# Optimization experiments

Measured on AMD Instinct MI355X. Metric: run time of the kernel, lower is better.

## Reference

```python
import jax, jax.numpy as jnp
import numpy as np

DIM = 240; NH = 6; HD = 20          # dim, num_heads, head_dim = dim // (2*num_heads)
WS = 16; BWS = 8                    # window size, base window size
R = (WS // BWS) ** 2                # spatial_linear in_features (=4)
LW = WS * WS; LB = BWS * BWS

# static relative-position index for a WSxWS window (same construction as torch buffer)
_coords = np.stack(np.meshgrid(np.arange(WS), np.arange(WS), indexing='ij')).reshape(2, -1)
_rel = (_coords[:, :, None] - _coords[:, None, :]).transpose(1, 2, 0).astype(np.int64)
_rel[..., 0] += WS - 1; _rel[..., 1] += WS - 1; _rel[..., 0] *= 2 * WS - 1
RPI = jnp.asarray(_rel.sum(-1))     # [LW, LW]


def conv2d(x, w, b, pad):
    y = jax.lax.conv_general_dilated(x, w, (1, 1), [(pad, pad), (pad, pad)],
                                     dimension_numbers=('NCHW', 'OIHW', 'NCHW'))
    return y + b[None, :, None, None]


def lrelu(x):
    return jnp.where(x >= 0, x, 0.2 * x)  # LeakyReLU(0.2)


def layer_norm(x, g, b, eps=1e-5):
    m = x.mean(-1, keepdims=True)
    v = jnp.mean((x - m) ** 2, axis=-1, keepdims=True)
    return (x - m) * jax.lax.rsqrt(v + eps) * g + b


def setup_inputs() -> dict:
    key = jax.random.key(0)
    ks = iter(jax.random.split(key, 40))
    rn = lambda shape: jax.random.normal(next(ks), shape, jnp.float32) * 0.02
    B, H, W = 2, 256, 256
    pd = (DIM // 4) // 4  # DynamicPosBias pos_dim = 15
    return {
        'x': jax.random.normal(next(ks), (B, H * W, DIM), jnp.float32),
        # DFE (qv projection)
        'c1_w': rn((DIM // 5, DIM, 1, 1)), 'c1_b': jnp.zeros((DIM // 5,), jnp.float32),
        'c2_w': rn((DIM // 5, DIM // 5, 3, 3)), 'c2_b': jnp.zeros((DIM // 5,), jnp.float32),
        'c3_w': rn((DIM, DIM // 5, 1, 1)), 'c3_b': jnp.zeros((DIM,), jnp.float32),
        'lin_w': rn((DIM, DIM, 1, 1)), 'lin_b': jnp.zeros((DIM,), jnp.float32),
        # spatial linear projection Linear(R, 1)
        'sl_w': rn((1, R)), 'sl_b': jnp.zeros((1,), jnp.float32),
        # DynamicPosBias MLP (residual=False)
        'pp_w': rn((pd, 2)), 'pp_b': jnp.zeros((pd,), jnp.float32),
        'ln1_g': jnp.ones((pd,), jnp.float32), 'ln1_b': jnp.zeros((pd,), jnp.float32),
        'p1_w': rn((pd, pd)), 'p1_b': jnp.zeros((pd,), jnp.float32),
        'ln2_g': jnp.ones((pd,), jnp.float32), 'ln2_b': jnp.zeros((pd,), jnp.float32),
        'p2_w': rn((pd, pd)), 'p2_b': jnp.zeros((pd,), jnp.float32),
        'ln3_g': jnp.ones((pd,), jnp.float32), 'ln3_b': jnp.zeros((pd,), jnp.float32),
        'p3_w': rn((NH, pd)), 'p3_b': jnp.zeros((NH,), jnp.float32),
        # output projection
        'proj_w': rn((DIM, DIM)), 'proj_b': jnp.zeros((DIM,), jnp.float32),
        'H': 256, 'W': 256,
    }


def reference(x, c1_w, c1_b, c2_w, c2_b, c3_w, c3_b, lin_w, lin_b, sl_w, sl_b,
              pp_w, pp_b, ln1_g, ln1_b, p1_w, p1_b, ln2_g, ln2_b, p2_w, p2_b,
              ln3_g, ln3_b, p3_w, p3_b, proj_w, proj_b, H, W):
    B, L, C = x.shape
    # ---- DFE feature projection (conv-gated) ----
    xi = jnp.transpose(x, (0, 2, 1)).reshape(B, C, H, W)
    conv = conv2d(lrelu(conv2d(lrelu(conv2d(xi, c1_w, c1_b, 0)), c2_w, c2_b, 1)), c3_w, c3_b, 0)
    qv = conv * conv2d(xi, lin_w, lin_b, 0)                       # [B,C,H,W]
    qv = jnp.transpose(qv, (0, 2, 3, 1))                          # [B,H,W,C]
    # ---- window partition ----
    nh_w, nw_w = H // WS, W // WS
    qv = qv.reshape(B, nh_w, WS, nw_w, WS, C).transpose(0, 1, 3, 2, 4, 5).reshape(-1, LW, C)
    B_ = qv.shape[0]
    qv = qv.reshape(B_, LW, 2, NH, HD).transpose(2, 0, 3, 1, 4)   # [2,B_,NH,LW,HD]
    q, v = qv[0], qv[1]
    # ---- spatial self-correlation ----
    # spatial linear projection of v: [B_,NH,LW,HD] -> [B_,NH,LB,HD]
    vs = v.reshape(B_, NH, BWS, WS // BWS, BWS, WS // BWS, HD)
    vs = vs.transpose(0, 1, 2, 4, 6, 3, 5).reshape(B_, NH, LB, HD, R)
    vs = jnp.einsum('bnkcr,or->bnkc', vs, sl_w) + sl_b            # Linear(R,1), squeezed
    corr = jnp.einsum('bnlc,bnkc->bnlk', q, vs) / HD              # [B_,NH,LW,LB]
    # dynamic relative position bias (MLP over the mother set of relative coords)
    ph = jnp.arange(1 - WS, WS)
    biases = jnp.stack(jnp.meshgrid(ph, ph, indexing='ij')).reshape(2, -1).T.astype(x.dtype)
    pos = biases @ pp_w.T + pp_b
    pos = jax.nn.relu(layer_norm(pos, ln1_g, ln1_b)) @ p1_w.T + p1_b
    pos = jax.nn.relu(layer_norm(pos, ln2_g, ln2_b)) @ p2_w.T + p2_b
    pos = jax.nn.relu(layer_norm(pos, ln3_g, ln3_b)) @ p3_w.T + p3_b  # [(2*WS-1)^2, NH]
    rpb = jnp.take(pos, RPI.reshape(-1), axis=0).reshape(LW, LW, NH).transpose(2, 0, 1)
    # pool key axis to base-window resolution (consistent with spatial_linear_projection grouping)
    rpb = rpb.reshape(NH, LW, BWS, WS // BWS, BWS, WS // BWS).mean((3, 5)).reshape(NH, LW, LB)
    corr = corr + rpb[None]
    x_s = jnp.einsum('bnlk,bnkc->bnlc', corr, vs)
    x_s = x_s.transpose(0, 2, 1, 3).reshape(B_, LW, NH * HD)      # [B_,LW,C/2]
    # ---- channel self-correlation (single-head over merged channels) ----
    qc = q.transpose(0, 2, 1, 3).reshape(B_, LW, NH * HD)
    vc = v.transpose(0, 2, 1, 3).reshape(B_, LW, NH * HD)
    corr_c = jnp.einsum('blc,bld->bcd', qc, vc) / LW              # [B_,C/2,C/2]
    x_c = jnp.einsum('bcd,bld->blc', corr_c, vc)                  # [B_,LW,C/2]
    # ---- window reverse + spatial-channel fusion ----
    def wrev(t):
        return t.reshape(B, nh_w, nw_w, WS, WS, -1).transpose(0, 1, 3, 2, 4, 5).reshape(B, H, W, -1)
    out = jnp.concatenate([wrev(x_s), wrev(x_c)], axis=-1)        # [B,H,W,C]
    out = out @ proj_w.T + proj_b
    return out.reshape(B, L, C)
```

## Files before the change

### kernel.cpp

```cpp
#include <hip/hip_runtime.h>
#include <math.h>

#define NPIX 131072

typedef __attribute__((ext_vector_type(8))) short bfrag;
typedef __attribute__((ext_vector_type(4))) float facc;
typedef __attribute__((ext_vector_type(4))) unsigned short us4;

__device__ __forceinline__ float lrelu_f(float x) { return x >= 0.f ? x : 0.2f * x; }

__device__ __forceinline__ int pix_of(int w, int l) {
    int b = w >> 8, wi = (w >> 4) & 15, wj = w & 15;
    return ((((b << 4) + wi) * 16 + (l >> 4)) << 8) + (wj << 4) + (l & 15);
}

__device__ __forceinline__ unsigned short bf16rn(float f) {
    unsigned u = __builtin_bit_cast(unsigned, f);
    u += 0x7FFFu + ((u >> 16) & 1u);
    return (unsigned short)(u >> 16);
}
__device__ __forceinline__ float bf16tof(unsigned short h) {
    unsigned u = ((unsigned)h) << 16;
    return __builtin_bit_cast(float, u);
}

__global__ __launch_bounds__(256) void split_x_kernel(const float* __restrict__ x,
                                                      unsigned short* __restrict__ xs2)
{
    int idx = blockIdx.x * 256 + threadIdx.x;
    int row = idx >> 5;
    int k = (idx & 31) * 8;
    float v[8];
    if (k < 240) {
        float4 a = *(const float4*)(x + (size_t)row * 240 + k);
        float4 b = *(const float4*)(x + (size_t)row * 240 + k + 4);
        v[0] = a.x; v[1] = a.y; v[2] = a.z; v[3] = a.w;
        v[4] = b.x; v[5] = b.y; v[6] = b.z; v[7] = b.w;
    } else {
#pragma unroll
        for (int e = 0; e < 8; ++e) v[e] = 0.f;
    }
    bfrag hi, lo;
#pragma unroll
    for (int e = 0; e < 8; ++e) {
        unsigned short h = bf16rn(v[e]);
        hi[e] = (short)h;
        lo[e] = (short)bf16rn(v[e] - bf16tof(h));
    }
    unsigned short* dst = xs2 + (size_t)row * 512 + k;
    *(bfrag*)(dst) = hi;
    *(bfrag*)(dst + 256) = lo;
}

__global__ __launch_bounds__(256) void pack_w_kernel(const float* __restrict__ src,
                                                     int rows, int K,
                                                     unsigned short* __restrict__ dst,
                                                     int total8, int KPAD)
{
    int idx = blockIdx.x * 256 + threadIdx.x;
    if (idx >= total8) return;
    int kper = KPAD >> 3;
    int row = idx / kper;
    int k = (idx - row * kper) * 8;
    float v[8];
#pragma unroll
    for (int e = 0; e < 8; ++e) {
        int kk = k + e;
        v[e] = (row < rows && kk < K) ? src[(size_t)row * K + kk] : 0.f;
    }
    bfrag hi, lo;
#pragma unroll
    for (int e = 0; e < 8; ++e) {
        unsigned short h = bf16rn(v[e]);
        hi[e] = (short)h;
        lo[e] = (short)bf16rn(v[e] - bf16tof(h));
    }
    unsigned short* d = dst + (size_t)row * 2 * KPAD + k;
    *(bfrag*)(d) = hi;
    *(bfrag*)(d + KPAD) = lo;
}

__global__ __launch_bounds__(256) void pack_c2w_kernel(const float* __restrict__ c2_w,
                                                       unsigned short* __restrict__ c2w2)
{
    int idx = blockIdx.x * 256 + threadIdx.x;
    if (idx >= 6912) return;
    int rowid = idx >> 4;
    int c = idx & 15;
    int tap = rowid / 48, n = rowid - tap * 48;
    int ty = tap / 3, tx = tap - ty * 3;
    int lohalf = c >> 3;
    int cbase = (c & 7) * 8;
    bfrag outv;
#pragma unroll
    for (int e = 0; e < 8; ++e) {
        int ci = cbase + e;
        float v = (ci < 48) ? c2_w[(((size_t)n * 48 + ci) * 3 + ty) * 3 + tx] : 0.f;
        unsigned short h = bf16rn(v);
        outv[e] = (short)(lohalf ? bf16rn(v - bf16tof(h)) : h);
    }
    *(bfrag*)(c2w2 + (size_t)rowid * 128 + c * 8) = outv;
}

__device__ __forceinline__ void ln_relu15(const float* h, float* r,
                                          const float* __restrict__ g,
                                          const float* __restrict__ b) {
    float m = 0.f;
#pragma unroll
    for (int f = 0; f < 15; ++f) m += h[f];
    m *= (1.f / 15.f);
    float v = 0.f;
#pragma unroll
    for (int f = 0; f < 15; ++f) { float d = h[f] - m; v += d * d; }
    float rs = rsqrtf(v * (1.f / 15.f) + 1e-5f);
#pragma unroll
    for (int f = 0; f < 15; ++f) {
        float xx = (h[f] - m) * rs * g[f] + b[f];
        r[f] = xx > 0.f ? xx : 0.f;
    }
}

__device__ __forceinline__ void lin15(const float* r, float* h,
                                      const float* __restrict__ w,
                                      const float* __restrict__ b) {
#pragma unroll
    for (int o = 0; o < 15; ++o) {
        float s = b[o];
#pragma unroll
        for (int g = 0; g < 15; ++g) s += r[g] * w[o * 15 + g];
        h[o] = s;
    }
}

__global__ __launch_bounds__(256) void prep_pos_kernel(
    const float* __restrict__ pp_w, const float* __restrict__ pp_b,
    const float* __restrict__ ln1_g, const float* __restrict__ ln1_b,
    const float* __restrict__ p1_w, const float* __restrict__ p1_b,
    const float* __restrict__ ln2_g, const float* __restrict__ ln2_b,
    const float* __restrict__ p2_w, const float* __restrict__ p2_b,
    const float* __restrict__ ln3_g, const float* __restrict__ ln3_b,
    const float* __restrict__ p3_w, const float* __restrict__ p3_b,
    float* __restrict__ pos3)
{
    int tid = threadIdx.x;
    for (int idx = tid; idx < 961; idx += 256) {
        float h[15], r[15];
        float in0 = (float)(idx / 31) - 15.f;
        float in1 = (float)(idx % 31) - 15.f;
#pragma unroll
        for (int f = 0; f < 15; ++f) h[f] = in0 * pp_w[2 * f] + in1 * pp_w[2 * f + 1] + pp_b[f];
        ln_relu15(h, r, ln1_g, ln1_b);
        lin15(r, h, p1_w, p1_b);
        ln_relu15(h, r, ln2_g, ln2_b);
        lin15(r, h, p2_w, p2_b);
        ln_relu15(h, r, ln3_g, ln3_b);
#pragma unroll
        for (int o = 0; o < 6; ++o) {
            float s = p3_b[o];
#pragma unroll
            for (int g = 0; g < 15; ++g) s += r[g] * p3_w[o * 15 + g];
            pos3[idx * 6 + o] = s;
        }
    }
}

__global__ __launch_bounds__(256) void rpb_kernel(const float* __restrict__ pos3,
                                                  float* __restrict__ rpb_t)
{
    int out = blockIdx.x * 256 + threadIdx.x;
    int n = out >> 14;
    int k = (out >> 8) & 63;
    int l = out & 255;
    int a = k >> 3, c = k & 7;
    int i1 = l >> 4, j1 = l & 15;
    float s = 0.f;
#pragma unroll
    for (int bb = 0; bb < 2; ++bb)
#pragma unroll
        for (int d = 0; d < 2; ++d) {
            int i2 = a * 2 + bb, j2 = c * 2 + d;
            int rpi = (i1 - i2 + 15) * 31 + (j1 - j2 + 15);
            s += pos3[rpi * 6 + n];
        }
    rpb_t[out] = s * 0.25f;
}

__device__ __forceinline__ void mfma_kpass3(const unsigned short* __restrict__ A2, int lda2,
                                            const unsigned short* __restrict__ W2, int ldw2,
                                            int ksteps, int mbase, int nbase,
                                            short* lds_a, short* lds_w,
                                            int tid, int wm, int wn,
                                            facc acc[4][4])
{
    int lane = tid & 63;
    int i = lane & 15, g = lane >> 4;
    int kpa = lda2 >> 1, kpw = ldw2 >> 1;
    for (int s = 0; s < ksteps; ++s) {
        int k0 = s * 32;
        {
            int r = tid >> 1, h16 = (tid & 1) * 16;
            const unsigned short* src = A2 + (size_t)(mbase + r) * lda2 + k0 + h16;
            bfrag h0 = *(const bfrag*)(src);
            bfrag h1 = *(const bfrag*)(src + 8);
            bfrag l0 = *(const bfrag*)(src + kpa);
            bfrag l1 = *(const bfrag*)(src + kpa + 8);
            short* dst = lds_a + r * 72 + h16;
            *(bfrag*)(dst)      = h0;  *(bfrag*)(dst + 8)  = h1;
            *(bfrag*)(dst + 32) = l0;  *(bfrag*)(dst + 40) = l1;
        }
        {
            int r = tid >> 1, half = tid & 1;
            const unsigned short* src = W2 + (size_t)(nbase + r) * ldw2 + half * kpw + k0;
            bfrag v0 = *(const bfrag*)(src);
            bfrag v1 = *(const bfrag*)(src + 8);
            bfrag v2 = *(const bfrag*)(src + 16);
            bfrag v3 = *(const bfrag*)(src + 24);
            short* dst = lds_w + r * 72 + half * 32;
            *(bfrag*)(dst)      = v0;  *(bfrag*)(dst + 8)  = v1;
            *(bfrag*)(dst + 16) = v2;  *(bfrag*)(dst + 24) = v3;
        }
        __syncthreads();
        bfrag ah[4], al[4], bh[4], bl[4];
#pragma unroll
        for (int mu = 0; mu < 4; ++mu) {
            const short* p = lds_a + (wm * 64 + mu * 16 + i) * 72 + g * 8;
            ah[mu] = *(const bfrag*)(p);
            al[mu] = *(const bfrag*)(p + 32);
        }
#pragma unroll
        for (int nu = 0; nu < 4; ++nu) {
            const short* p = lds_w + (wn * 64 + nu * 16 + i) * 72 + g * 8;
            bh[nu] = *(const bfrag*)(p);
            bl[nu] = *(const bfrag*)(p + 32);
        }
#pragma unroll
        for (int mu = 0; mu < 4; ++mu)
#pragma unroll
            for (int nu = 0; nu < 4; ++nu) {
                acc[mu][nu] = __builtin_amdgcn_mfma_f32_16x16x32_bf16(ah[mu], bh[nu], acc[mu][nu], 0, 0, 0);
                acc[mu][nu] = __builtin_amdgcn_mfma_f32_16x16x32_bf16(ah[mu], bl[nu], acc[mu][nu], 0, 0, 0);
                acc[mu][nu] = __builtin_amdgcn_mfma_f32_16x16x32_bf16(al[mu], bh[nu], acc[mu][nu], 0, 0, 0);
            }
        __syncthreads();
    }
}

__global__ __launch_bounds__(256) void conv1_mfma_kernel(const unsigned short* __restrict__ xs2,
    const unsigned short* __restrict__ c1_w2, const float* __restrict__ bias,
    unsigned short* __restrict__ t1s)
{
    __shared__ __align__(16) short lds_a[128 * 72];
    __shared__ __align__(16) short lds_w[128 * 72];
    int tid = threadIdx.x;
    int lane = tid & 63, wid = tid >> 6;
    int wm = wid >> 1, wn = wid & 1;
    int mbase = blockIdx.x * 128;
    facc zero = {0.f, 0.f, 0.f, 0.f};
    facc acc[4][4];
#pragma unroll
    for (int mu = 0; mu < 4; ++mu)
#pragma unroll
        for (int nu = 0; nu < 4; ++nu) acc[mu][nu] = zero;

    mfma_kpass3(xs2, 512, c1_w2, 512, 8, mbase, 0, lds_a, lds_w, tid, wm, wn, acc);

    int i = lane & 15, g = lane >> 4;
#pragma unroll
    for (int nu = 0; nu < 4; ++nu) {
        int n = wn * 64 + nu * 16 + i;
        if (n < 48) {
            float bv = bias[n];
#pragma unroll
            for (int mu = 0; mu < 4; ++mu)
#pragma unroll
                for (int rr = 0; rr < 4; ++rr) {
                    size_t m = (size_t)mbase + wm * 64 + mu * 16 + g * 4 + rr;
                    float v = lrelu_f(acc[mu][nu][rr] + bv);
                    unsigned short h = bf16rn(v);
                    t1s[m * 128 + n] = h;
                    t1s[m * 128 + 64 + n] = bf16rn(v - bf16tof(h));
                }
        }
    }
    if (tid < 128) {
        size_t m = (size_t)mbase + tid;
        bfrag z = {0, 0, 0, 0, 0, 0, 0, 0};
        *(bfrag*)(t1s + m * 128 + 48)  = z;
        *(bfrag*)(t1s + m * 128 + 56)  = z;
        *(bfrag*)(t1s + m * 128 + 112) = z;
        *(bfrag*)(t1s + m * 128 + 120) = z;
    }
}

__global__ __launch_bounds__(256) void conv2_mfma_kernel(const unsigned short* __restrict__ t1s,
    const unsigned short* __restrict__ c2w2, const float* __restrict__ bias,
    unsigned short* __restrict__ t2s)
{
    __shared__ __align__(16) short a_s[130 * 128];
    int bid = blockIdx.x;
    int b = bid >> 9;
    int r = (bid >> 1) & 255;
    int half = bid & 1;
    int c0 = half * 128;
    int tid = threadIdx.x;
    int lane = tid & 63, wid = tid >> 6;
    int i = lane & 15, g = lane >> 4;
    facc zero = {0.f, 0.f, 0.f, 0.f};
    facc acc[2][3];
#pragma unroll
    for (int mu = 0; mu < 2; ++mu)
#pragma unroll
        for (int nu = 0; nu < 3; ++nu) acc[mu][nu] = zero;

    for (int dy = 0; dy < 3; ++dy) {
        int grow = r + dy - 1;
        bool rowok = (grow >= 0 && grow < 256);
        for (int idx = tid; idx < 130 * 16; idx += 256) {
            int j = idx >> 4, ch = idx & 15;
            int gc = c0 - 1 + j;
            bfrag v = {0, 0, 0, 0, 0, 0, 0, 0};
            if (rowok && gc >= 0 && gc < 256) {
                size_t gpix = ((size_t)b * 256 + grow) * 256 + gc;
                v = *(const bfrag*)(t1s + gpix * 128 + ch * 8);
            }
            *(bfrag*)&a_s[j * 128 + ((ch ^ (j & 7)) * 8)] = v;
        }
        __syncthreads();
#pragma unroll
        for (int dx = 0; dx < 3; ++dx) {
            const unsigned short* wb = c2w2 + (size_t)(dy * 3 + dx) * 48 * 128;
#pragma unroll
            for (int h = 0; h < 2; ++h) {
                bfrag ah[2], al[2], bh[3], bl[3];
#pragma unroll
                for (int mu = 0; mu < 2; ++mu) {
                    int j = wid * 32 + mu * 16 + i + dx;
                    int chi = (h * 4 + g) ^ (j & 7);
                    int clo = (8 + h * 4 + g) ^ (j & 7);
                    ah[mu] = *(const bfrag*)&a_s[j * 128 + chi * 8];
                    al[mu] = *(const bfrag*)&a_s[j * 128 + clo * 8];
                }
#pragma unroll
                for (int nu = 0; nu < 3; ++nu) {
                    const unsigned short* wp = wb + (size_t)(nu * 16 + i) * 128 + h * 32 + g * 8;
                    bh[nu] = *(const bfrag*)(wp);
                    bl[nu] = *(const bfrag*)(wp + 64);
                }
#pragma unroll
                for (int mu = 0; mu < 2; ++mu)
#pragma unroll
                    for (int nu = 0; nu < 3; ++nu) {
                        acc[mu][nu] = __builtin_amdgcn_mfma_f32_16x16x32_bf16(ah[mu], bh[nu], acc[mu][nu], 0, 0, 0);
                        acc[mu][nu] = __builtin_amdgcn_mfma_f32_16x16x32_bf16(ah[mu], bl[nu], acc[mu][nu], 0, 0, 0);
                        acc[mu][nu] = __builtin_amdgcn_mfma_f32_16x16x32_bf16(al[mu], bh[nu], acc[mu][nu], 0, 0, 0);
                    }
            }
        }
        __syncthreads();
    }
#pragma unroll
    for (int nu = 0; nu < 3; ++nu) {
        int n = nu * 16 + i;
        float bv = bias[n];
#pragma unroll
        for (int mu = 0; mu < 2; ++mu)
#pragma unroll
            for (int rr = 0; rr < 4; ++rr) {
                int lp = wid * 32 + mu * 16 + g * 4 + rr;
                size_t gpix = ((size_t)b * 256 + r) * 256 + (c0 + lp);
                float v = lrelu_f(acc[mu][nu][rr] + bv);
                unsigned short h = bf16rn(v);
                t2s[gpix * 128 + n] = h;
                t2s[gpix * 128 + 64 + n] = bf16rn(v - bf16tof(h));
            }
    }
    if (tid < 128) {
        size_t gpix = ((size_t)b * 256 + r) * 256 + (c0 + tid);
        bfrag z = {0, 0, 0, 0, 0, 0, 0, 0};
        *(bfrag*)(t2s + gpix * 128 + 48)  = z;
        *(bfrag*)(t2s + gpix * 128 + 56)  = z;
        *(bfrag*)(t2s + gpix * 128 + 112) = z;
        *(bfrag*)(t2s + gpix * 128 + 120) = z;
    }
}

__global__ __launch_bounds__(256) void qv_mfma_kernel(const unsigned short* __restrict__ xs2,
    const unsigned short* __restrict__ lin_w2, const float* __restrict__ lin_b,
    const unsigned short* __restrict__ t2s, const unsigned short* __restrict__ c3_w2,
    const float* __restrict__ c3_b, float* __restrict__ qv)
{
    __shared__ __align__(16) short lds_a[128 * 72];
    __shared__ __align__(16) short lds_w[128 * 72];
    int tid = threadIdx.x;
    int lane = tid & 63, wid = tid >> 6;
    int wm = wid >> 1, wn = wid & 1;
    int bid = blockIdx.y * 2 + blockIdx.x;
    int xcd = bid & 7, j = bid >> 3;
    int mbase = (xcd * 128 + (j >> 1)) * 128;
    int nbase = (j & 1) * 128;
    facc zero = {0.f, 0.f, 0.f, 0.f};
    facc acc1[4][4], acc2[4][4];
#pragma unroll
    for (int mu = 0; mu < 4; ++mu)
#pragma unroll
        for (int nu = 0; nu < 4; ++nu) { acc1[mu][nu] = zero; acc2[mu][nu] = zero; }

    mfma_kpass3(xs2, 512, lin_w2, 512, 8, mbase, nbase, lds_a, lds_w, tid, wm, wn, acc1);
    mfma_kpass3(t2s, 128, c3_w2, 128, 2, mbase, nbase, lds_a, lds_w, tid, wm, wn, acc2);

    int i = lane & 15, g = lane >> 4;
#pragma unroll
    for (int nu = 0; nu < 4; ++nu) {
        int n = nbase + wn * 64 + nu * 16 + i;
        if (n < 240) {
            float lb = lin_b[n], cb = c3_b[n];
#pragma unroll
            for (int mu = 0; mu < 4; ++mu)
#pragma unroll
                for (int rr = 0; rr < 4; ++rr) {
                    size_t m = (size_t)mbase + wm * 64 + mu * 16 + g * 4 + rr;
                    qv[m * 240 + n] = (acc2[mu][nu][rr] + cb) * (acc1[mu][nu][rr] + lb);
                }
        }
    }
}

__global__ __launch_bounds__(256) void proj_mfma_kernel(const unsigned short* __restrict__ cat2,
    const unsigned short* __restrict__ proj_w2, const float* __restrict__ bias,
    float* __restrict__ out)
{
    __shared__ __align__(16) short lds_a[128 * 72];
    __shared__ __align__(16) short lds_w[128 * 72];
    int tid = threadIdx.x;
    int lane = tid & 63, wid = tid >> 6;
    int wm = wid >> 1, wn = wid & 1;
    int bid = blockIdx.y * 2 + blockIdx.x;
    int xcd = bid & 7, j = bid >> 3;
    int mbase = (xcd * 128 + (j >> 1)) * 128;
    int nbase = (j & 1) * 128;
    facc zero = {0.f, 0.f, 0.f, 0.f};
    facc acc[4][4];
#pragma unroll
    for (int mu = 0; mu < 4; ++mu)
#pragma unroll
        for (int nu = 0; nu < 4; ++nu) acc[mu][nu] = zero;

    mfma_kpass3(cat2, 512, proj_w2, 512, 8, mbase, nbase, lds_a, lds_w, tid, wm, wn, acc);

    int i = lane & 15, g = lane >> 4;
#pragma unroll
    for (int nu = 0; nu < 4; ++nu) {
        int n = nbase + wn * 64 + nu * 16 + i;
        if (n < 240) {
            float bv = bias[n];
#pragma unroll
            for (int mu = 0; mu < 4; ++mu)
#pragma unroll
                for (int rr = 0; rr < 4; ++rr) {
                    size_t m = (size_t)mbase + wm * 64 + mu * 16 + g * 4 + rr;
                    out[m * 240 + n] = acc[mu][nu][rr] + bv;
                }
        }
    }
}

__global__ __launch_bounds__(256) void xs_kernel(const float* __restrict__ qv,
    const float* __restrict__ rpb_t, const float* __restrict__ sl_w,
    const float* __restrict__ sl_b, unsigned short* __restrict__ cat2)
{
    __shared__ __align__(16) float v_s[256 * 20];
    __shared__ __align__(16) float vs_s[64 * 20];
    int bid = blockIdx.x;
    int xcd = bid & 7;
    int j = bid >> 3;
    int wl = j / 6;
    int n = j - wl * 6;
    int w = xcd * 64 + wl;
    int tid = threadIdx.x;
    int l = tid;
    size_t pix = (size_t)pix_of(w, l);
    const float* qp = qv + pix * 240 + n * 20;
    float qr[20];
#pragma unroll
    for (int h4 = 0; h4 < 5; ++h4) {
        *(float4*)&qr[h4 * 4] = *(const float4*)(qp + h4 * 4);
        *(float4*)&v_s[l * 20 + h4 * 4] = *(const float4*)(qp + 120 + h4 * 4);
    }
    __syncthreads();
    float slw0 = sl_w[0], slw1 = sl_w[1], slw2 = sl_w[2], slw3 = sl_w[3];
    float slb = sl_b[0];
    for (int idx = tid; idx < 1280; idx += 256) {
        int k = idx / 20, hd = idx % 20;
        int a = k >> 3, c = k & 7;
        int l00 = a * 32 + c * 2;
        float vsum = slb
                   + slw0 * v_s[(l00 + 0) * 20 + hd]
                   + slw1 * v_s[(l00 + 1) * 20 + hd]
                   + slw2 * v_s[(l00 + 16) * 20 + hd]
                   + slw3 * v_s[(l00 + 17) * 20 + hd];
        vs_s[idx] = vsum;
    }
    __syncthreads();
    const float* rp = rpb_t + (size_t)n * 16384 + l;
    float acc[20];
#pragma unroll
    for (int hd = 0; hd < 20; ++hd) acc[hd] = 0.f;
#pragma unroll
    for (int k = 0; k < 64; ++k) {
        float vr[20];
#pragma unroll
        for (int h4 = 0; h4 < 5; ++h4)
            *(float4*)&vr[h4 * 4] = *(const float4*)&vs_s[k * 20 + h4 * 4];
        float s0 = 0.f, s1 = 0.f, s2 = 0.f, s3 = 0.f;
#pragma unroll
        for (int hd = 0; hd < 20; hd += 4) {
            s0 += qr[hd + 0] * vr[hd + 0];
            s1 += qr[hd + 1] * vr[hd + 1];
            s2 += qr[hd + 2] * vr[hd + 2];
            s3 += qr[hd + 3] * vr[hd + 3];
        }
        float cc = (s0 + s1 + s2 + s3) * (1.f / 20.f) + rp[(size_t)k * 256];
#pragma unroll
        for (int hd = 0; hd < 20; ++hd) acc[hd] += cc * vr[hd];
    }
    unsigned short* op = cat2 + pix * 512 + n * 20;
#pragma unroll
    for (int h4 = 0; h4 < 5; ++h4) {
        us4 h, lo;
#pragma unroll
        for (int e = 0; e < 4; ++e) {
            float v = acc[h4 * 4 + e];
            unsigned short hh = bf16rn(v);
            h[e] = hh;
            lo[e] = bf16rn(v - bf16tof(hh));
        }
        *(us4*)(op + h4 * 4) = h;
        *(us4*)(op + 256 + h4 * 4) = lo;
    }
    if (n == 0) {
        bfrag z = {0, 0, 0, 0, 0, 0, 0, 0};
        unsigned short* zp = cat2 + pix * 512;
        *(bfrag*)(zp + 240) = z;  *(bfrag*)(zp + 248) = z;
        *(bfrag*)(zp + 496) = z;  *(bfrag*)(zp + 504) = z;
    }
}

__global__ __launch_bounds__(256) void corrc_kernel(const float* __restrict__ qv,
                                                    float* __restrict__ G)
{
    __shared__ __align__(16) float vc_s[16 * 124];
    __shared__ __align__(16) float qc_s[16 * 124];
    int bid = blockIdx.x;
    int w = (bid & 7) * 64 + (bid >> 3);
    int tid = threadIdx.x, ty = tid >> 4, tx = tid & 15;
    float acc[8][8] = {};
    for (int l0 = 0; l0 < 256; l0 += 16) {
        for (int idx = tid; idx < 480; idx += 256) {
            int k = idx / 30, c4 = idx % 30;
            size_t pix = (size_t)pix_of(w, l0 + k);
            const float* qp = qv + pix * 240;
            *(float4*)&qc_s[k * 124 + c4 * 4] = *(const float4*)(qp + c4 * 4);
            *(float4*)&vc_s[k * 124 + c4 * 4] = *(const float4*)(qp + 120 + c4 * 4);
        }
        __syncthreads();
#pragma unroll
        for (int k = 0; k < 16; ++k) {
            float4 a0 = *(const float4*)&vc_s[k * 124 + ty * 8];
            float4 a1 = *(const float4*)&vc_s[k * 124 + ty * 8 + 4];
            float4 b0 = *(const float4*)&qc_s[k * 124 + tx * 8];
            float4 b1 = *(const float4*)&qc_s[k * 124 + tx * 8 + 4];
            float av[8] = {a0.x, a0.y, a0.z, a0.w, a1.x, a1.y, a1.z, a1.w};
            float bv[8] = {b0.x, b0.y, b0.z, b0.w, b1.x, b1.y, b1.z, b1.w};
#pragma unroll
            for (int i = 0; i < 8; ++i)
#pragma unroll
                for (int j = 0; j < 8; ++j) acc[i][j] += av[i] * bv[j];
        }
        __syncthreads();
    }
    float* gp = G + (size_t)w * 14400;
#pragma unroll
    for (int i = 0; i < 8; ++i) {
        int d = ty * 8 + i;
        if (d < 120) {
#pragma unroll
            for (int j4 = 0; j4 < 2; ++j4) {
                int c = tx * 8 + j4 * 4;
                if (c < 120) {
                    float4 o;
                    o.x = acc[i][j4 * 4 + 0]; o.y = acc[i][j4 * 4 + 1];
                    o.z = acc[i][j4 * 4 + 2]; o.w = acc[i][j4 * 4 + 3];
                    *(float4*)(gp + (size_t)d * 120 + c) = o;
                }
            }
        }
    }
}

__global__ __launch_bounds__(256) void xc_kernel(const float* __restrict__ qv,
    const float* __restrict__ G, unsigned short* __restrict__ cat2)
{
    __shared__ __align__(16) float a_s[8 * 132];
    __shared__ __align__(16) float b_s[8 * 124];
    int bid = blockIdx.x;
    int xcd = bid & 7, j = bid >> 3;
    int w = xcd * 64 + (j >> 1);
    int mh = j & 1;
    int tid = threadIdx.x, ty = tid >> 4, tx = tid & 15;
    const float* gp = G + (size_t)w * 14400;
    float acc[8][8] = {};
    for (int k0 = 0; k0 < 120; k0 += 8) {
        {
            int lloc = tid >> 1;
            int kk = (tid & 1) * 4;
            int l = mh * 128 + lloc;
            size_t pix = (size_t)pix_of(w, l);
            float4 v = *(const float4*)(qv + pix * 240 + 120 + k0 + kk);
            a_s[(kk + 0) * 132 + lloc] = v.x;
            a_s[(kk + 1) * 132 + lloc] = v.y;
            a_s[(kk + 2) * 132 + lloc] = v.z;
            a_s[(kk + 3) * 132 + lloc] = v.w;
        }
        if (tid < 240) {
            int k = tid / 30, c4 = tid % 30;
            *(float4*)&b_s[k * 124 + c4 * 4] =
                *(const float4*)(gp + (size_t)(k0 + k) * 120 + c4 * 4);
        }
        __syncthreads();
#pragma unroll
        for (int k = 0; k < 8; ++k) {
            float4 a0 = *(const float4*)&a_s[k * 132 + ty * 8];
            float4 a1 = *(const float4*)&a_s[k * 132 + ty * 8 + 4];
            float4 b0 = *(const float4*)&b_s[k * 124 + tx * 8];
            float4 b1 = *(const float4*)&b_s[k * 124 + tx * 8 + 4];
            float av[8] = {a0.x, a0.y, a0.z, a0.w, a1.x, a1.y, a1.z, a1.w};
            float bv[8] = {b0.x, b0.y, b0.z, b0.w, b1.x, b1.y, b1.z, b1.w};
#pragma unroll
            for (int i = 0; i < 8; ++i)
#pragma unroll
                for (int j2 = 0; j2 < 8; ++j2) acc[i][j2] += av[i] * bv[j2];
        }
        __syncthreads();
    }
#pragma unroll
    for (int i = 0; i < 8; ++i) {
        int l = mh * 128 + ty * 8 + i;
        size_t pix = (size_t)pix_of(w, l);
        unsigned short* op = cat2 + pix * 512;
#pragma unroll
        for (int j4 = 0; j4 < 2; ++j4) {
            int c = tx * 8 + j4 * 4;
            if (c < 120) {
                us4 h, lo;
#pragma unroll
                for (int e = 0; e < 4; ++e) {
                    float v = acc[i][j4 * 4 + e] * (1.f / 256.f);
                    unsigned short hh = bf16rn(v);
                    h[e] = hh;
                    lo[e] = bf16rn(v - bf16tof(hh));
                }
                *(us4*)(op + 120 + c) = h;
                *(us4*)(op + 256 + 120 + c) = lo;
            }
        }
    }
}

extern "C" void kernel_launch(void* const* d_in, const int* in_sizes, int n_in,
                              void* d_out, int out_size, void* d_ws, size_t ws_size,
                              hipStream_t stream)
{
    (void)in_sizes; (void)n_in; (void)out_size;
    const float* x     = (const float*)d_in[0];
    const float* c1_w  = (const float*)d_in[1];
    const float* c1_b  = (const float*)d_in[2];
    const float* c2_w  = (const float*)d_in[3];
    const float* c2_b  = (const float*)d_in[4];
    const float* c3_w  = (const float*)d_in[5];
    const float* c3_b  = (const float*)d_in[6];
    const float* lin_w = (const float*)d_in[7];
    const float* lin_b = (const float*)d_in[8];
    const float* sl_w  = (const float*)d_in[9];
    const float* sl_b  = (const float*)d_in[10];
    const float* pp_w  = (const float*)d_in[11];
    const float* pp_b  = (const float*)d_in[12];
    const float* ln1_g = (const float*)d_in[13];
    const float* ln1_b = (const float*)d_in[14];
    const float* p1_w  = (const float*)d_in[15];
    const float* p1_b  = (const float*)d_in[16];
    const float* ln2_g = (const float*)d_in[17];
    const float* ln2_b = (const float*)d_in[18];
    const float* p2_w  = (const float*)d_in[19];
    const float* p2_b  = (const float*)d_in[20];
    const float* ln3_g = (const float*)d_in[21];
    const float* ln3_b = (const float*)d_in[22];
    const float* p3_w  = (const float*)d_in[23];
    const float* p3_b  = (const float*)d_in[24];
    const float* proj_w = (const float*)d_in[25];
    const float* proj_b = (const float*)d_in[26];

    float* ws = (float*)d_ws;
    float* pos3   = ws;
    float* rpb_t  = ws + 8192;
    unsigned short* lin_w2  = (unsigned short*)(ws + 106496);
    unsigned short* c3_w2   = (unsigned short*)(ws + 172032);
    unsigned short* proj_w2 = (unsigned short*)(ws + 188416);
    unsigned short* c1_w2   = (unsigned short*)(ws + 253952);
    unsigned short* c2w2    = (unsigned short*)(ws + 286720);
    unsigned short* t2s = (unsigned short*)(ws + 314368);
    float* G      = ws + 314368;
    unsigned short* xs2 = (unsigned short*)(ws + 8702976);
    unsigned short* cat2 = xs2;
    float* qvb    = ws + 42257408;
    unsigned short* t1s = (unsigned short*)qvb;
    const size_t required = (size_t)73714688 * 4;
    if (ws_size < required) return;

    pack_w_kernel<<<32, 256, 0, stream>>>(lin_w, 240, 240, lin_w2, 256 * 32, 256);
    pack_w_kernel<<<32, 256, 0, stream>>>(proj_w, 240, 240, proj_w2, 256 * 32, 256);
    pack_w_kernel<<<8, 256, 0, stream>>>(c3_w, 240, 48, c3_w2, 256 * 8, 64);
    pack_w_kernel<<<16, 256, 0, stream>>>(c1_w, 48, 240, c1_w2, 128 * 32, 256);
    pack_c2w_kernel<<<27, 256, 0, stream>>>(c2_w, c2w2);
    split_x_kernel<<<16384, 256, 0, stream>>>(x, xs2);
    prep_pos_kernel<<<1, 256, 0, stream>>>(pp_w, pp_b, ln1_g, ln1_b, p1_w, p1_b,
                                           ln2_g, ln2_b, p2_w, p2_b, ln3_g, ln3_b,
                                           p3_w, p3_b, pos3);
    rpb_kernel<<<384, 256, 0, stream>>>(pos3, rpb_t);
    conv1_mfma_kernel<<<1024, 256, 0, stream>>>(xs2, c1_w2, c1_b, t1s);
    conv2_mfma_kernel<<<1024, 256, 0, stream>>>(t1s, c2w2, c2_b, t2s);
    qv_mfma_kernel<<<dim3(2, 1024), 256, 0, stream>>>(xs2, lin_w2, lin_b, t2s, c3_w2, c3_b, qvb);
    xs_kernel<<<3072, 256, 0, stream>>>(qvb, rpb_t, sl_w, sl_b, cat2);
    corrc_kernel<<<512, 256, 0, stream>>>(qvb, G);
    xc_kernel<<<1024, 256, 0, stream>>>(qvb, G, cat2);
    proj_mfma_kernel<<<dim3(2, 1024), 256, 0, stream>>>(cat2, proj_w2, proj_b, (float*)d_out);
}
```

Before: 608.7 us.

## Register-prefetch next K tile in MFMA loops and shrink conv1 N-tile to 64

The shared MFMA k-loop now loads the next K-step's A and W fragments into registers before computing the current step, then writes them to LDS after a barrier. This overlaps global loads with MFMA work. A new 64-column variant is used for conv1, whose output has only 48 channels, so the old 128-wide tile wasted MFMA work and LDS on padded columns. Each iteration now has two barriers instead of one and holds more registers for the prefetched fragments.

```diff
diff --git a/kernel.cpp b/kernel.cpp
--- a/kernel.cpp
+++ b/kernel.cpp
@@ -195,31 +195,33 @@
     int lane = tid & 63;
     int i = lane & 15, g = lane >> 4;
     int kpa = lda2 >> 1, kpw = ldw2 >> 1;
+    int ra = tid >> 1, h16 = (tid & 1) * 16;
+    const unsigned short* srcA = A2 + (size_t)(mbase + ra) * lda2 + h16;
+    short* dstA = lds_a + ra * 72 + h16;
+    int halfw = tid & 1;
+    const unsigned short* srcW = W2 + (size_t)(nbase + ra) * ldw2 + halfw * kpw;
+    short* dstW = lds_w + ra * 72 + halfw * 32;
+
+    bfrag pa0, pa1, pa2, pa3, pw0, pw1, pw2, pw3;
+    pa0 = *(const bfrag*)(srcA);       pa1 = *(const bfrag*)(srcA + 8);
+    pa2 = *(const bfrag*)(srcA + kpa); pa3 = *(const bfrag*)(srcA + kpa + 8);
+    pw0 = *(const bfrag*)(srcW);       pw1 = *(const bfrag*)(srcW + 8);
+    pw2 = *(const bfrag*)(srcW + 16);  pw3 = *(const bfrag*)(srcW + 24);
+    *(bfrag*)(dstA)      = pa0;  *(bfrag*)(dstA + 8)  = pa1;
+    *(bfrag*)(dstA + 32) = pa2;  *(bfrag*)(dstA + 40) = pa3;
+    *(bfrag*)(dstW)      = pw0;  *(bfrag*)(dstW + 8)  = pw1;
+    *(bfrag*)(dstW + 16) = pw2;  *(bfrag*)(dstW + 24) = pw3;
+    __syncthreads();
+
     for (int s = 0; s < ksteps; ++s) {
-        int k0 = s * 32;
-        {
-            int r = tid >> 1, h16 = (tid & 1) * 16;
-            const unsigned short* src = A2 + (size_t)(mbase + r) * lda2 + k0 + h16;
-            bfrag h0 = *(const bfrag*)(src);
-            bfrag h1 = *(const bfrag*)(src + 8);
-            bfrag l0 = *(const bfrag*)(src + kpa);
-            bfrag l1 = *(const bfrag*)(src + kpa + 8);
-            short* dst = lds_a + r * 72 + h16;
-            *(bfrag*)(dst)      = h0;  *(bfrag*)(dst + 8)  = h1;
-            *(bfrag*)(dst + 32) = l0;  *(bfrag*)(dst + 40) = l1;
-        }
-        {
-            int r = tid >> 1, half = tid & 1;
-            const unsigned short* src = W2 + (size_t)(nbase + r) * ldw2 + half * kpw + k0;
-            bfrag v0 = *(const bfrag*)(src);
-            bfrag v1 = *(const bfrag*)(src + 8);
-            bfrag v2 = *(const bfrag*)(src + 16);
-            bfrag v3 = *(const bfrag*)(src + 24);
-            short* dst = lds_w + r * 72 + half * 32;
-            *(bfrag*)(dst)      = v0;  *(bfrag*)(dst + 8)  = v1;
-            *(bfrag*)(dst + 16) = v2;  *(bfrag*)(dst + 24) = v3;
-        }
-        __syncthreads();
+        bool more = (s + 1 < ksteps);
+        int k1 = (s + 1) * 32;
+        if (more) {
+            pa0 = *(const bfrag*)(srcA + k1);       pa1 = *(const bfrag*)(srcA + k1 + 8);
+            pa2 = *(const bfrag*)(srcA + kpa + k1); pa3 = *(const bfrag*)(srcA + kpa + k1 + 8);
+            pw0 = *(const bfrag*)(srcW + k1);       pw1 = *(const bfrag*)(srcW + k1 + 8);
+            pw2 = *(const bfrag*)(srcW + k1 + 16);  pw3 = *(const bfrag*)(srcW + k1 + 24);
+        }
         bfrag ah[4], al[4], bh[4], bl[4];
 #pragma unroll
         for (int mu = 0; mu < 4; ++mu) {
@@ -242,6 +244,92 @@
                 acc[mu][nu] = __builtin_amdgcn_mfma_f32_16x16x32_bf16(al[mu], bh[nu], acc[mu][nu], 0, 0, 0);
             }
         __syncthreads();
+        if (more) {
+            *(bfrag*)(dstA)      = pa0;  *(bfrag*)(dstA + 8)  = pa1;
+            *(bfrag*)(dstA + 32) = pa2;  *(bfrag*)(dstA + 40) = pa3;
+            *(bfrag*)(dstW)      = pw0;  *(bfrag*)(dstW + 8)  = pw1;
+            *(bfrag*)(dstW + 16) = pw2;  *(bfrag*)(dstW + 24) = pw3;
+        }
+        __syncthreads();
+    }
+}
+
+__device__ __forceinline__ void mfma_kpass_n64(const unsigned short* __restrict__ A2, int lda2,
+                                               const unsigned short* __restrict__ W2, int ldw2,
+                                               int ksteps, int mbase,
+                                               short* lds_a, short* lds_w,
+                                               int tid, int wm, int wn,
+                                               facc acc[4][2])
+{
+    int lane = tid & 63;
+    int i = lane & 15, g = lane >> 4;
+    int kpa = lda2 >> 1, kpw = ldw2 >> 1;
+    int ra = tid >> 1, h16 = (tid & 1) * 16;
+    const unsigned short* srcA = A2 + (size_t)(mbase + ra) * lda2 + h16;
+    short* dstA = lds_a + ra * 72 + h16;
+    bool wok = (tid < 128);
+    int rw = tid >> 1;
+    int halfw = tid & 1;
+    const unsigned short* srcW = W2 + (size_t)rw * ldw2 + halfw * kpw;
+    short* dstW = lds_w + rw * 72 + halfw * 32;
+
+    bfrag pa0, pa1, pa2, pa3, pw0 = {}, pw1 = {}, pw2 = {}, pw3 = {};
+    pa0 = *(const bfrag*)(srcA);       pa1 = *(const bfrag*)(srcA + 8);
+    pa2 = *(const bfrag*)(srcA + kpa); pa3 = *(const bfrag*)(srcA + kpa + 8);
+    if (wok) {
+        pw0 = *(const bfrag*)(srcW);       pw1 = *(const bfrag*)(srcW + 8);
+        pw2 = *(const bfrag*)(srcW + 16);  pw3 = *(const bfrag*)(srcW + 24);
+    }
+    *(bfrag*)(dstA)      = pa0;  *(bfrag*)(dstA + 8)  = pa1;
+    *(bfrag*)(dstA + 32) = pa2;  *(bfrag*)(dstA + 40) = pa3;
+    if (wok) {
+        *(bfrag*)(dstW)      = pw0;  *(bfrag*)(dstW + 8)  = pw1;
+        *(bfrag*)(dstW + 16) = pw2;  *(bfrag*)(dstW + 24) = pw3;
+    }
+    __syncthreads();
+
+    for (int s = 0; s < ksteps; ++s) {
+        bool more = (s + 1 < ksteps);
+        int k1 = (s + 1) * 32;
+        if (more) {
+            pa0 = *(const bfrag*)(srcA + k1);       pa1 = *(const bfrag*)(srcA + k1 + 8);
+            pa2 = *(const bfrag*)(srcA + kpa + k1); pa3 = *(const bfrag*)(srcA + kpa + k1 + 8);
+            if (wok) {
+                pw0 = *(const bfrag*)(srcW + k1);       pw1 = *(const bfrag*)(srcW + k1 + 8);
+                pw2 = *(const bfrag*)(srcW + k1 + 16);  pw3 = *(const bfrag*)(srcW + k1 + 24);
+            }
+        }
+        bfrag ah[4], al[4], bh[2], bl[2];
+#pragma unroll
+        for (int mu = 0; mu < 4; ++mu) {
+            const short* p = lds_a + (wm * 64 + mu * 16 + i) * 72 + g * 8;
+            ah[mu] = *(const bfrag*)(p);
+            al[mu] = *(const bfrag*)(p + 32);
+        }
+#pragma unroll
+        for (int nu = 0; nu < 2; ++nu) {
+            const short* p = lds_w + (wn * 32 + nu * 16 + i) * 72 + g * 8;
+            bh[nu] = *(const bfrag*)(p);
+            bl[nu] = *(const bfrag*)(p + 32);
+        }
+#pragma unroll
+        for (int mu = 0; mu < 4; ++mu)
+#pragma unroll
+            for (int nu = 0; nu < 2; ++nu) {
+                acc[mu][nu] = __builtin_amdgcn_mfma_f32_16x16x32_bf16(ah[mu], bh[nu], acc[mu][nu], 0, 0, 0);
+                acc[mu][nu] = __builtin_amdgcn_mfma_f32_16x16x32_bf16(ah[mu], bl[nu], acc[mu][nu], 0, 0, 0);
+                acc[mu][nu] = __builtin_amdgcn_mfma_f32_16x16x32_bf16(al[mu], bh[nu], acc[mu][nu], 0, 0, 0);
+            }
+        __syncthreads();
+        if (more) {
+            *(bfrag*)(dstA)      = pa0;  *(bfrag*)(dstA + 8)  = pa1;
+            *(bfrag*)(dstA + 32) = pa2;  *(bfrag*)(dstA + 40) = pa3;
+            if (wok) {
+                *(bfrag*)(dstW)      = pw0;  *(bfrag*)(dstW + 8)  = pw1;
+                *(bfrag*)(dstW + 16) = pw2;  *(bfrag*)(dstW + 24) = pw3;
+            }
+        }
+        __syncthreads();
     }
 }
 
@@ -250,24 +338,24 @@
     unsigned short* __restrict__ t1s)
 {
     __shared__ __align__(16) short lds_a[128 * 72];
-    __shared__ __align__(16) short lds_w[128 * 72];
+    __shared__ __align__(16) short lds_w[64 * 72];
     int tid = threadIdx.x;
     int lane = tid & 63, wid = tid >> 6;
     int wm = wid >> 1, wn = wid & 1;
     int mbase = blockIdx.x * 128;
     facc zero = {0.f, 0.f, 0.f, 0.f};
-    facc acc[4][4];
+    facc acc[4][2];
 #pragma unroll
     for (int mu = 0; mu < 4; ++mu)
 #pragma unroll
-        for (int nu = 0; nu < 4; ++nu) acc[mu][nu] = zero;
-
-    mfma_kpass3(xs2, 512, c1_w2, 512, 8, mbase, 0, lds_a, lds_w, tid, wm, wn, acc);
+        for (int nu = 0; nu < 2; ++nu) acc[mu][nu] = zero;
+
+    mfma_kpass_n64(xs2, 512, c1_w2, 512, 8, mbase, lds_a, lds_w, tid, wm, wn, acc);
 
     int i = lane & 15, g = lane >> 4;
 #pragma unroll
-    for (int nu = 0; nu < 4; ++nu) {
-        int n = wn * 64 + nu * 16 + i;
+    for (int nu = 0; nu < 2; ++nu) {
+        int n = wn * 32 + nu * 16 + i;
         if (n < 48) {
             float bv = bias[n];
 #pragma unroll
```

Result: slower. 643.7 us (+5.8%).
